# Performance work log

Measured on AMD Instinct MI355X. Metric: run time of the kernel, lower is better.

## Reference

```python
import jax, jax.numpy as jnp
import numpy as np

BN_EPS = 1e-5


def adder2d(x, w, stride=1, padding=1):
    """AdderNet layer: out[b,o,h,w] = -sum_{c,kh,kw} |patch - w|.
    x: [B,C,H,W], w: [O,C,K,K] -> [B,O,Ho,Wo]."""
    B, C, H, W = x.shape
    O, _, K, _ = w.shape
    # patches: [B, C*K*K, Ho, Wo] (feature order = (C, Kh, Kw), matching w.reshape)
    patches = jax.lax.conv_general_dilated_patches(
        x, (K, K), (stride, stride), [(padding, padding), (padding, padding)])
    Bp, F, Ho, Wo = patches.shape
    Xm = patches.transpose(0, 2, 3, 1).reshape(-1, F)  # [N, F], N = B*Ho*Wo
    Wm = w.reshape(O, F)
    # loop over output channels (O small) to avoid a [N, O, F] intermediate
    out = jax.lax.map(lambda wo: -jnp.sum(jnp.abs(Xm - wo), axis=-1), Wm)  # [O, N]
    return out.reshape(O, B, Ho, Wo).transpose(1, 0, 2, 3)


def batchnorm2d(x, gamma, beta):
    # training-mode BN: batch statistics over (B, H, W)
    mean = jnp.mean(x, axis=(0, 2, 3), keepdims=True)
    var = jnp.var(x, axis=(0, 2, 3), keepdims=True)
    inv = jax.lax.rsqrt(var + BN_EPS)
    return (x - mean) * inv * gamma[None, :, None, None] + beta[None, :, None, None]


def setup_inputs() -> dict:
    key = jax.random.key(0)
    ks = jax.random.split(key, 5)
    x = jax.random.normal(ks[0], (256, 1, 64, 64), dtype=jnp.float32)
    w1 = jax.random.normal(ks[1], (16, 1, 3, 3), dtype=jnp.float32) * 0.3
    w2 = jax.random.normal(ks[2], (32, 16, 3, 3), dtype=jnp.float32) * 0.1
    g1 = jnp.ones((16,), jnp.float32); b1 = jnp.zeros((16,), jnp.float32)
    g2 = jnp.ones((32,), jnp.float32); b2 = jnp.zeros((32,), jnp.float32)
    fc_w = jax.random.normal(ks[3], (10, 32), dtype=jnp.float32) * 0.1
    fc_b = jnp.zeros((10,), jnp.float32)
    return {"x": x, "w1": w1, "g1": g1, "b1": b1, "w2": w2,
            "g2": g2, "b2": b2, "fc_w": fc_w, "fc_b": fc_b}


def reference(x, w1, g1, b1, w2, g2, b2, fc_w, fc_b):
    h = jax.nn.relu(batchnorm2d(adder2d(x, w1), g1, b1))   # [B,16,64,64]
    h = jax.nn.relu(batchnorm2d(adder2d(h, w2), g2, b2))   # [B,32,64,64]
    h = jnp.mean(h, axis=(2, 3))                            # adaptive avg pool -> [B,32]
    return h @ fc_w.T + fc_b                                # [B,10]
```

## Files before the change

### kernel.cpp

```cpp
#include <hip/hip_runtime.h>
#include <hip/hip_fp16.h>


#define HW 4096

typedef unsigned int u32;
typedef unsigned long long u64;
typedef unsigned short u16;
typedef unsigned char u8;
typedef __attribute__((ext_vector_type(4))) unsigned int u32x4;

__device__ __forceinline__ u32x4 mqsad(u64 src, u32 ref, u32x4 acc) {
#if __has_builtin(__builtin_amdgcn_mqsad_u32_u8)
  return __builtin_amdgcn_mqsad_u32_u8(src, ref, acc);
#else
  u32x4 d;
  asm("v_mqsad_u32_u8 %0, %1, %2, %3"
      : "=&v"(d)
      : "v"(src), "v"(ref), "v"(acc));
  return d;
#endif
}

__device__ __forceinline__ u32 q8(float v) {
  return (u32)fminf(fmaxf(fmaf(v, 32.f, 128.5f), 0.f), 255.f);
}

__global__ __launch_bounds__(512, 4) void k_stats1(const float* __restrict__ x,
                                                   const float* __restrict__ w1,
                                                   double* __restrict__ s1,
                                                   const float* __restrict__ w2,
                                                   u32* __restrict__ w2b,
                                                   u16* __restrict__ y1) {
  __shared__ __align__(16) u8 sxt[2720];
  __shared__ __align__(16) u32 w1r[48];
  __shared__ u32 redu[128];
  int blk = blockIdx.x, tid = threadIdx.x;
  int b = blk >> 1, ih = blk & 1;
  int R0 = ih << 5;

  if (blk == 0) {
    int oc = tid >> 4, c = tid & 15;
    int og = oc >> 3, o = oc & 7;
    const float* wp = w2 + (oc * 16 + c) * 9;
    u32 q[9];
#pragma unroll
    for (int t = 0; t < 9; t++) {
      float qf = rintf(fmaf(wp[t], 32.f, 48.f));
      q[t] = (u32)fminf(fmaxf(qf, 1.f), 255.f);
    }
    u32* dst = w2b + ((og * 16 + c) * 8 + o) * 3;
    dst[0] = q[0] | (q[1] << 8) | (q[2] << 16);
    dst[1] = q[3] | (q[4] << 8) | (q[5] << 16);
    dst[2] = q[6] | (q[7] << 8) | (q[8] << 16);
  }

  const float* xb = x + b * HW;
  for (int i = tid; i < 2720; i += 512) {
    int row = i / 80, col = i - row * 80;
    int ry = R0 + row - 1, rx = col - 1;
    float xv = (ry >= 0 && ry < 64 && rx >= 0 && rx < 64) ? xb[ry * 64 + rx] : 0.f;
    sxt[i] = (u8)q8(xv);
  }
  if (tid < 48) {
    int c = tid / 3, dy = tid - c * 3;
    const float* wp = w1 + c * 9 + dy * 3;
    w1r[tid] = q8(wp[0]) | (q8(wp[1]) << 8) | (q8(wp[2]) << 16);
  }
  __syncthreads();

  int chh = tid >> 8;
  int t8 = tid & 255;
  int r = t8 >> 3;
  int x0 = (t8 & 7) << 3;
  u32 ref[8][3];
  {
    const u32x4* rl = (const u32x4*)(w1r + chh * 24);
    u32x4 v0 = rl[0], v1 = rl[1], v2 = rl[2], v3 = rl[3], v4 = rl[4], v5 = rl[5];
    ref[0][0] = v0.x; ref[0][1] = v0.y; ref[0][2] = v0.z;
    ref[1][0] = v0.w; ref[1][1] = v1.x; ref[1][2] = v1.y;
    ref[2][0] = v1.z; ref[2][1] = v1.w; ref[2][2] = v2.x;
    ref[3][0] = v2.y; ref[3][1] = v2.z; ref[3][2] = v2.w;
    ref[4][0] = v3.x; ref[4][1] = v3.y; ref[4][2] = v3.z;
    ref[5][0] = v3.w; ref[5][1] = v4.x; ref[5][2] = v4.y;
    ref[6][0] = v4.z; ref[6][1] = v4.w; ref[6][2] = v5.x;
    ref[7][0] = v5.y; ref[7][1] = v5.z; ref[7][2] = v5.w;
  }
  const u8* rp = sxt + r * 80 + x0;
  u64 lo0 = *(const u64*)(rp);
  u32 M0 = *(const u32*)(rp + 8);
  u64 lo1 = *(const u64*)(rp + 80);
  u32 M1 = *(const u32*)(rp + 88);
  u64 lo2 = *(const u64*)(rp + 160);
  u32 M2 = *(const u32*)(rp + 168);
  u64 hi0 = (lo0 >> 32) | ((u64)M0 << 32);
  u64 hi1 = (lo1 >> 32) | ((u64)M1 << 32);
  u64 hi2 = (lo2 >> 32) | ((u64)M2 << 32);
  u32 ssum[8], ssq[8];
  u32x4 z = (u32x4)(0u);
#pragma unroll
  for (int cl = 0; cl < 8; cl++) {
    int c = chh * 8 + cl;
    u32x4 ql = mqsad(lo2, ref[cl][2],
               mqsad(lo1, ref[cl][1], mqsad(lo0, ref[cl][0], z)));
    u32x4 qh = mqsad(hi2, ref[cl][2],
               mqsad(hi1, ref[cl][1], mqsad(hi0, ref[cl][0], z)));
    ssum[cl] = ql.x + ql.y + ql.z + ql.w + qh.x + qh.y + qh.z + qh.w;
    ssq[cl] = ql.x * ql.x + ql.y * ql.y + ql.z * ql.z + ql.w * ql.w +
              qh.x * qh.x + qh.y * qh.y + qh.z * qh.z + qh.w * qh.w;
    uint4 st = make_uint4(ql.x | (ql.y << 16), ql.z | (ql.w << 16),
                          qh.x | (qh.y << 16), qh.z | (qh.w << 16));
    *(uint4*)(y1 + (((size_t)(b * 16 + c)) << 12) + ((R0 + r) << 6) + x0) = st;
  }
  int lane = tid & 63, wv = tid >> 6;
#pragma unroll
  for (int cl = 0; cl < 8; cl++) {
    u32 s = ssum[cl], q = ssq[cl];
    for (int off = 32; off; off >>= 1) {
      s += (u32)__shfl_down((int)s, off, 64);
      q += (u32)__shfl_down((int)q, off, 64);
    }
    if (lane == 0) { redu[(wv * 8 + cl) * 2] = s; redu[(wv * 8 + cl) * 2 + 1] = q; }
  }
  __syncthreads();
  if (tid < 16) {
    int ch2 = tid >> 3, cl = tid & 7;
    double sd = 0.0, qd = 0.0;
#pragma unroll
    for (int w = 0; w < 4; w++) {
      sd += (double)redu[((ch2 * 4 + w) * 8 + cl) * 2];
      qd += (double)redu[((ch2 * 4 + w) * 8 + cl) * 2 + 1];
    }
    atomicAdd(&s1[tid], -sd * (1.0 / 32.0));
    atomicAdd(&s1[16 + tid], qd * (1.0 / 1024.0));
  }
}

__global__ __launch_bounds__(512, 6) void k_layer2(
    const u16* __restrict__ y1, const double* __restrict__ s1,
    const float* __restrict__ g1, const float* __restrict__ b1,
    const u32* __restrict__ w2b, __half* __restrict__ a2,
    double* __restrict__ s2) {
  __shared__ __align__(16) u8 shu[16 * 1440];
  __shared__ float red[8 * 8];
  __shared__ float p1a[16], p1b[16];
  int blk = blockIdx.x;
  int b = blk >> 2, Y0 = (blk & 3) << 4;
  int tid = threadIdx.x;

  if (tid < 16) {
    double N = 1048576.0;
    double mean = s1[tid] / N;
    double var = s1[16 + tid] / N - mean * mean;
    float inv = (float)(1.0 / sqrt(var + 1e-5));
    float sc = g1[tid] * inv;
    float sf = b1[tid] - (float)mean * sc;
    p1a[tid] = -sc;
    p1b[tid] = fmaf(sf, 32.f, 48.5f);
  }
  __syncthreads();

  for (int jj = tid; jj < 2304; jj += 512) {
    int rowjob = jj >> 3, kq = jj & 7;
    int ch = rowjob / 18;
    int rr = rowjob - ch * 18;
    int gr = Y0 + rr - 1;
    float pa8 = p1a[ch], pb8 = p1b[ch];
    u32 B[8];
    if (gr >= 0 && gr < 64) {
      uint4 v = *(const uint4*)(
          y1 + (((size_t)(b * 16 + ch)) << 12) + (gr << 6) + (kq << 3));
      const u32* vd = (const u32*)&v;
#pragma unroll
      for (int qq = 0; qq < 4; qq++) {
        float t0 = fmaf((float)(vd[qq] & 0xffffu), pa8, pb8);
        float t1 = fmaf((float)(vd[qq] >> 16), pa8, pb8);
        B[qq * 2] = (u32)fminf(fmaxf(t0, 48.5f), 255.f);
        B[qq * 2 + 1] = (u32)fminf(fmaxf(t1, 48.5f), 255.f);
      }
    } else {
#pragma unroll
      for (int qq = 0; qq < 8; qq++) B[qq] = 48u;
    }
    u32 prev = (u32)__shfl_up((int)B[7], 1, 64);
    if (kq == 0) prev = 48u;
    u32 d0 = prev | (B[0] << 8) | (B[1] << 16) | (B[2] << 24);
    u32 d1 = B[3] | (B[4] << 8) | (B[5] << 16) | (B[6] << 24);
    u8* dst = shu + ch * 1440 + rr * 80 + (kq << 3);
    *(uint2*)dst = make_uint2(d0, d1);
    if (kq == 7)
      *(u32*)(dst + 8) = B[7] | 0x30303000u;
  }
  __syncthreads();

  int lane = tid & 63;
  int w8 = tid >> 6;
  int og = w8 >> 1, half = w8 & 1;
  int wofs = __builtin_amdgcn_readfirstlane(og * 384 + half * 12);
  const u32* wbase = w2b + wofs;
  int rb = lane >> 3;
  int x0 = (lane & 7) << 3;

  float ssumB[4], ssqB[4];
#pragma unroll
  for (int o = 0; o < 4; o++) { ssumB[o] = 0.f; ssqB[o] = 0.f; }

#pragma unroll 1
  for (int pr = 0; pr < 2; pr++) {
    int y0 = Y0 + pr * 8;
    const u8* shb = shu + (pr * 8 + rb) * 80 + x0;

    u32x4 acc[4][2];
#pragma unroll
    for (int o = 0; o < 4; o++) { acc[o][0] = (u32x4)(0u); acc[o][1] = (u32x4)(0u); }

    u64 Aa[3], Ab[3];
    u32 Ma[3], Mb[3];
    u32 Wa[12], Wb[12];

#define LOADC(Av, Mv, Wv, cc)                                     \
  do {                                                            \
    const u8* rp_ = shb + (cc) * 1440;                            \
    _Pragma("unroll") for (int dy_ = 0; dy_ < 3; dy_++) {         \
      Av[dy_] = *(const u64*)(rp_ + dy_ * 80);                    \
      Mv[dy_] = *(const u32*)(rp_ + dy_ * 80 + 8);                \
    }                                                             \
    const u32* wc_ = wbase + (cc) * 24;                           \
    _Pragma("unroll") for (int j_ = 0; j_ < 12; j_++) Wv[j_] = wc_[j_]; \
  } while (0)

#define COMPUTE(Av, Mv, Wv)                                       \
  do {                                                            \
    _Pragma("unroll") for (int dy_ = 0; dy_ < 3; dy_++) {         \
      u64 lo_ = Av[dy_];                                          \
      u64 hi_ = (Av[dy_] >> 32) | ((u64)Mv[dy_] << 32);           \
      _Pragma("unroll") for (int o_ = 0; o_ < 4; o_++) {          \
        u32 wr_ = Wv[o_ * 3 + dy_];                               \
        acc[o_][0] = mqsad(lo_, wr_, acc[o_][0]);                 \
        acc[o_][1] = mqsad(hi_, wr_, acc[o_][1]);                 \
      }                                                           \
    }                                                             \
  } while (0)

    LOADC(Aa, Ma, Wa, 0);
#pragma unroll 1
    for (int c = 0; c < 16; c += 2) {
      LOADC(Ab, Mb, Wb, c + 1);
      COMPUTE(Aa, Ma, Wa);
      if (c < 14) LOADC(Aa, Ma, Wa, c + 2);
      COMPUTE(Ab, Mb, Wb);
    }
#undef LOADC
#undef COMPUTE

    const float ksc = -1.f / 32.f;
    __half* a2b =
        a2 + ((size_t)b * 32 + og * 8 + half * 4) * HW + (y0 + rb) * 64 + x0;
#pragma unroll
    for (int o = 0; o < 4; o++) {
      float f0 = (float)acc[o][0].x * ksc, f1 = (float)acc[o][0].y * ksc;
      float f2 = (float)acc[o][0].z * ksc, f3 = (float)acc[o][0].w * ksc;
      float f4 = (float)acc[o][1].x * ksc, f5 = (float)acc[o][1].y * ksc;
      float f6 = (float)acc[o][1].z * ksc, f7 = (float)acc[o][1].w * ksc;
      __half2 h01 = __floats2half2_rn(f0, f1);
      __half2 h23 = __floats2half2_rn(f2, f3);
      __half2 h45 = __floats2half2_rn(f4, f5);
      __half2 h67 = __floats2half2_rn(f6, f7);
      uint4 st = make_uint4(*(u32*)&h01, *(u32*)&h23, *(u32*)&h45, *(u32*)&h67);
      *(uint4*)(a2b + o * HW) = st;
      float2 c0 = __half22float2(h01), c1 = __half22float2(h23);
      float2 c2 = __half22float2(h45), c3 = __half22float2(h67);
      ssumB[o] += c0.x + c0.y + c1.x + c1.y + c2.x + c2.y + c3.x + c3.y;
      ssqB[o] += c0.x * c0.x + c0.y * c0.y + c1.x * c1.x + c1.y * c1.y +
                 c2.x * c2.x + c2.y * c2.y + c3.x * c3.x + c3.y * c3.y;
    }
  }

#pragma unroll
  for (int o = 0; o < 4; o++) {
    float s = ssumB[o], q = ssqB[o];
    for (int off = 32; off; off >>= 1) {
      s += __shfl_down(s, off, 64);
      q += __shfl_down(q, off, 64);
    }
    if (lane == 0) { red[w8 * 8 + o * 2] = s; red[w8 * 8 + o * 2 + 1] = q; }
  }
  __syncthreads();
  if (tid < 32) {
    int oc = tid;
    int ww = (oc >> 3) * 2 + ((oc >> 2) & 1);
    int oo = oc & 3;
    atomicAdd(&s2[oc], (double)red[ww * 8 + oo * 2]);
    atomicAdd(&s2[32 + oc], (double)red[ww * 8 + oo * 2 + 1]);
  }
}

__global__ __launch_bounds__(512) void k_poolfc(const __half* __restrict__ a2,
                                                const double* __restrict__ s2,
                                                const float* __restrict__ g2,
                                                const float* __restrict__ b2,
                                                const float* __restrict__ fw,
                                                const float* __restrict__ fb,
                                                float* __restrict__ out) {
  __shared__ float sc2s[16], sf2s[16];
  __shared__ float poolv[16];
  int blk = blockIdx.x, tid = threadIdx.x;
  int b = blk >> 1, hh = blk & 1;
  if (tid < 16) {
    int oc = hh * 16 + tid;
    double N = 1048576.0;
    double mean = s2[oc] / N;
    double var = s2[32 + oc] / N - mean * mean;
    float inv = (float)(1.0 / sqrt(var + 1e-5));
    float sc = g2[oc] * inv;
    sc2s[tid] = sc;
    sf2s[tid] = b2[oc] - (float)mean * sc;
  }
  __syncthreads();
  int o = tid >> 5, part = tid & 31;
  int oc = hh * 16 + o;
  const uint4* p = (const uint4*)(a2 + ((size_t)b * 32 + oc) * HW);
  float s = sc2s[o], f = sf2s[o];
  float acc = 0.f;
#pragma unroll
  for (int i = 0; i < 16; i++) {
    uint4 v = p[i * 32 + part];
    float2 f0 = __half22float2(*(const __half2*)&v.x);
    float2 f1 = __half22float2(*(const __half2*)&v.y);
    float2 f2 = __half22float2(*(const __half2*)&v.z);
    float2 f3 = __half22float2(*(const __half2*)&v.w);
    acc += fmaxf(fmaf(f0.x, s, f), 0.f) + fmaxf(fmaf(f0.y, s, f), 0.f) +
           fmaxf(fmaf(f1.x, s, f), 0.f) + fmaxf(fmaf(f1.y, s, f), 0.f) +
           fmaxf(fmaf(f2.x, s, f), 0.f) + fmaxf(fmaf(f2.y, s, f), 0.f) +
           fmaxf(fmaf(f3.x, s, f), 0.f) + fmaxf(fmaf(f3.y, s, f), 0.f);
  }
  acc += __shfl_down(acc, 16, 32);
  acc += __shfl_down(acc, 8, 32);
  acc += __shfl_down(acc, 4, 32);
  acc += __shfl_down(acc, 2, 32);
  acc += __shfl_down(acc, 1, 32);
  if (part == 0) poolv[o] = acc * (1.f / 4096.f);
  __syncthreads();
  if (tid < 10) {
    float rr = 0.f;
#pragma unroll
    for (int j = 0; j < 16; j++) rr += poolv[j] * fw[tid * 32 + hh * 16 + j];
    if (hh == 0) rr += fb[tid];
    atomicAdd(&out[b * 10 + tid], rr);
  }
}

extern "C" void kernel_launch(void* const* d_in, const int* in_sizes, int n_in,
                              void* d_out, int out_size, void* d_ws, size_t ws_size,
                              hipStream_t stream) {
  const float* x   = (const float*)d_in[0];
  const float* w1  = (const float*)d_in[1];
  const float* g1  = (const float*)d_in[2];
  const float* b1  = (const float*)d_in[3];
  const float* w2  = (const float*)d_in[4];
  const float* g2  = (const float*)d_in[5];
  const float* b2  = (const float*)d_in[6];
  const float* fcw = (const float*)d_in[7];
  const float* fcb = (const float*)d_in[8];
  float* out = (float*)d_out;

  char* ws = (char*)d_ws;
  __half* a2 = (__half*)ws;
  double* stats = (double*)(ws + 67108864);
  double* s1 = stats;
  double* s2 = stats + 32;
  u32* w2b = (u32*)(ws + 67108864 + 1024);
  u16* y1 = (u16*)(ws + 67108864 + 16384);

  hipMemsetAsync(stats, 0, 768, stream);
  k_stats1<<<512, 512, 0, stream>>>(x, w1, s1, w2, w2b, y1);
  k_layer2<<<1024, 512, 0, stream>>>(y1, s1, g1, b1, w2b, a2, s2);
  k_poolfc<<<512, 512, 0, stream>>>(a2, s2, g2, b2, fcw, fcb, out);
}
```

Before: 175.3 us.

## Widen per-lane tile to 16 pixels and drop the two-pass row loop

Each lane now computes 16 consecutive output pixels of one row (4 lanes per row, 16 rows per wave) instead of 8 pixels over two 8-row passes. The loop over passes is removed, so each channel's shared-memory rows and weights are loaded once per block instead of twice, and the 16-byte loads give more mqsad work per load. In exchange the accumulators double to 16 u32x4 per lane, so launch bounds drop from 6 to 4 blocks per CU, which lowers occupancy.

```diff
diff --git a/kernel.cpp b/kernel.cpp
--- a/kernel.cpp
+++ b/kernel.cpp
@@ -136,7 +136,7 @@
   }
 }
 
-__global__ __launch_bounds__(512, 6) void k_layer2(
+__global__ __launch_bounds__(512, 4) void k_layer2(
     const u16* __restrict__ y1, const double* __restrict__ s1,
     const float* __restrict__ g1, const float* __restrict__ b1,
     const u32* __restrict__ w2b, __half* __restrict__ a2,
@@ -198,32 +198,26 @@
   int og = w8 >> 1, half = w8 & 1;
   int wofs = __builtin_amdgcn_readfirstlane(og * 384 + half * 12);
   const u32* wbase = w2b + wofs;
-  int rb = lane >> 3;
-  int x0 = (lane & 7) << 3;
-
-  float ssumB[4], ssqB[4];
-#pragma unroll
-  for (int o = 0; o < 4; o++) { ssumB[o] = 0.f; ssqB[o] = 0.f; }
-
-#pragma unroll 1
-  for (int pr = 0; pr < 2; pr++) {
-    int y0 = Y0 + pr * 8;
-    const u8* shb = shu + (pr * 8 + rb) * 80 + x0;
-
-    u32x4 acc[4][2];
-#pragma unroll
-    for (int o = 0; o < 4; o++) { acc[o][0] = (u32x4)(0u); acc[o][1] = (u32x4)(0u); }
-
-    u64 Aa[3], Ab[3];
-    u32 Ma[3], Mb[3];
-    u32 Wa[12], Wb[12];
+  int r = lane >> 2;
+  int cg = lane & 3;
+  const u8* shb = shu + r * 80 + cg * 16;
+
+  u32x4 acc[4][4];
+#pragma unroll
+  for (int o = 0; o < 4; o++)
+#pragma unroll
+    for (int qd = 0; qd < 4; qd++) acc[o][qd] = (u32x4)(0u);
+
+  u32x4 Aa[3], Ab[3];
+  u32 Ma[3], Mb[3];
+  u32 Wa[12], Wb[12];
 
 #define LOADC(Av, Mv, Wv, cc)                                     \
   do {                                                            \
     const u8* rp_ = shb + (cc) * 1440;                            \
     _Pragma("unroll") for (int dy_ = 0; dy_ < 3; dy_++) {         \
-      Av[dy_] = *(const u64*)(rp_ + dy_ * 80);                    \
-      Mv[dy_] = *(const u32*)(rp_ + dy_ * 80 + 8);                \
+      Av[dy_] = *(const u32x4*)(rp_ + dy_ * 80);                  \
+      Mv[dy_] = *(const u32*)(rp_ + dy_ * 80 + 16);               \
     }                                                             \
     const u32* wc_ = wbase + (cc) * 24;                           \
     _Pragma("unroll") for (int j_ = 0; j_ < 12; j_++) Wv[j_] = wc_[j_]; \
@@ -232,48 +226,78 @@
 #define COMPUTE(Av, Mv, Wv)                                       \
   do {                                                            \
     _Pragma("unroll") for (int dy_ = 0; dy_ < 3; dy_++) {         \
-      u64 lo_ = Av[dy_];                                          \
-      u64 hi_ = (Av[dy_] >> 32) | ((u64)Mv[dy_] << 32);           \
+      u32x4 D_ = Av[dy_];                                         \
+      u64 s0_ = (u64)D_.x | ((u64)D_.y << 32);                    \
+      u64 s1_ = (u64)D_.y | ((u64)D_.z << 32);                    \
+      u64 s2_ = (u64)D_.z | ((u64)D_.w << 32);                    \
+      u64 s3_ = (u64)D_.w | ((u64)Mv[dy_] << 32);                 \
       _Pragma("unroll") for (int o_ = 0; o_ < 4; o_++) {          \
         u32 wr_ = Wv[o_ * 3 + dy_];                               \
-        acc[o_][0] = mqsad(lo_, wr_, acc[o_][0]);                 \
-        acc[o_][1] = mqsad(hi_, wr_, acc[o_][1]);                 \
+        acc[o_][0] = mqsad(s0_, wr_, acc[o_][0]);                 \
+        acc[o_][1] = mqsad(s1_, wr_, acc[o_][1]);                 \
+        acc[o_][2] = mqsad(s2_, wr_, acc[o_][2]);                 \
+        acc[o_][3] = mqsad(s3_, wr_, acc[o_][3]);                 \
       }                                                           \
     }                                                             \
   } while (0)
 
-    LOADC(Aa, Ma, Wa, 0);
+  LOADC(Aa, Ma, Wa, 0);
 #pragma unroll 1
-    for (int c = 0; c < 16; c += 2) {
-      LOADC(Ab, Mb, Wb, c + 1);
-      COMPUTE(Aa, Ma, Wa);
-      if (c < 14) LOADC(Aa, Ma, Wa, c + 2);
-      COMPUTE(Ab, Mb, Wb);
-    }
+  for (int c = 0; c < 16; c += 2) {
+    LOADC(Ab, Mb, Wb, c + 1);
+    COMPUTE(Aa, Ma, Wa);
+    if (c < 14) LOADC(Aa, Ma, Wa, c + 2);
+    COMPUTE(Ab, Mb, Wb);
+  }
 #undef LOADC
 #undef COMPUTE
 
-    const float ksc = -1.f / 32.f;
-    __half* a2b =
-        a2 + ((size_t)b * 32 + og * 8 + half * 4) * HW + (y0 + rb) * 64 + x0;
-#pragma unroll
-    for (int o = 0; o < 4; o++) {
-      float f0 = (float)acc[o][0].x * ksc, f1 = (float)acc[o][0].y * ksc;
-      float f2 = (float)acc[o][0].z * ksc, f3 = (float)acc[o][0].w * ksc;
-      float f4 = (float)acc[o][1].x * ksc, f5 = (float)acc[o][1].y * ksc;
-      float f6 = (float)acc[o][1].z * ksc, f7 = (float)acc[o][1].w * ksc;
-      __half2 h01 = __floats2half2_rn(f0, f1);
-      __half2 h23 = __floats2half2_rn(f2, f3);
-      __half2 h45 = __floats2half2_rn(f4, f5);
-      __half2 h67 = __floats2half2_rn(f6, f7);
-      uint4 st = make_uint4(*(u32*)&h01, *(u32*)&h23, *(u32*)&h45, *(u32*)&h67);
-      *(uint4*)(a2b + o * HW) = st;
-      float2 c0 = __half22float2(h01), c1 = __half22float2(h23);
-      float2 c2 = __half22float2(h45), c3 = __half22float2(h67);
-      ssumB[o] += c0.x + c0.y + c1.x + c1.y + c2.x + c2.y + c3.x + c3.y;
-      ssqB[o] += c0.x * c0.x + c0.y * c0.y + c1.x * c1.x + c1.y * c1.y +
-                 c2.x * c2.x + c2.y * c2.y + c3.x * c3.x + c3.y * c3.y;
-    }
+  const float ksc = -1.f / 32.f;
+  float ssumB[4], ssqB[4];
+  __half* a2b =
+      a2 + ((size_t)b * 32 + og * 8 + half * 4) * HW + (Y0 + r) * 64 + cg * 16;
+#pragma unroll
+  for (int o = 0; o < 4; o++) {
+    float f[16];
+#pragma unroll
+    for (int qd = 0; qd < 4; qd++) {
+      f[qd * 4 + 0] = (float)acc[o][qd].x * ksc;
+      f[qd * 4 + 1] = (float)acc[o][qd].y * ksc;
+      f[qd * 4 + 2] = (float)acc[o][qd].z * ksc;
+      f[qd * 4 + 3] = (float)acc[o][qd].w * ksc;
+    }
+    uint4 st0, st1;
+    {
+      __half2 h0 = __floats2half2_rn(f[0], f[1]);
+      __half2 h1 = __floats2half2_rn(f[2], f[3]);
+      __half2 h2 = __floats2half2_rn(f[4], f[5]);
+      __half2 h3 = __floats2half2_rn(f[6], f[7]);
+      __half2 h4 = __floats2half2_rn(f[8], f[9]);
+      __half2 h5 = __floats2half2_rn(f[10], f[11]);
+      __half2 h6 = __floats2half2_rn(f[12], f[13]);
+      __half2 h7 = __floats2half2_rn(f[14], f[15]);
+      st0 = make_uint4(*(u32*)&h0, *(u32*)&h1, *(u32*)&h2, *(u32*)&h3);
+      st1 = make_uint4(*(u32*)&h4, *(u32*)&h5, *(u32*)&h6, *(u32*)&h7);
+    }
+    *(uint4*)(a2b + o * HW) = st0;
+    *(uint4*)(a2b + o * HW + 8) = st1;
+    float s = 0.f, q = 0.f;
+    const u32* sw = (const u32*)&st0;
+#pragma unroll
+    for (int j = 0; j < 4; j++) {
+      float2 fc = __half22float2(*(const __half2*)&sw[j]);
+      s += fc.x + fc.y;
+      q += fc.x * fc.x + fc.y * fc.y;
+    }
+    const u32* sw1 = (const u32*)&st1;
+#pragma unroll
+    for (int j = 0; j < 4; j++) {
+      float2 fc = __half22float2(*(const __half2*)&sw1[j]);
+      s += fc.x + fc.y;
+      q += fc.x * fc.x + fc.y * fc.y;
+    }
+    ssumB[o] = s;
+    ssqB[o] = q;
   }
 
 #pragma unroll
```

After: 178.8 us. About the same (+2.0%).
